# Optimization experiments

Hardware: AMD Instinct MI355X
Metric: run time of the kernel (lower is better)

Reference implementation:

```python
import jax, jax.numpy as jnp
import numpy as np

DIM = 192
TDIM = 192
HEADS = 6
WS = (2, 7, 7)
SS = (1, 3, 3)
MLP_HID = 4 * DIM
RANK = DIM // 8
EPS = 1e-6


def _rel_pos_index(ws):
    wd, wh, ww = ws
    coords = np.stack(np.meshgrid(np.arange(wd), np.arange(wh), np.arange(ww), indexing='ij'))
    cf = coords.reshape(3, -1)
    rel = (cf[:, :, None] - cf[:, None, :]).transpose(1, 2, 0).astype(np.int64)
    rel[..., 0] += wd - 1
    rel[..., 1] += wh - 1
    rel[..., 2] += ww - 1
    rel[..., 0] *= (2 * wh - 1) * (2 * ww - 1)
    rel[..., 1] *= (2 * ww - 1)
    return rel.sum(-1)  # (N, N)


def _window_partition(x, ws):
    B, D, H, W, C = x.shape
    x = x.reshape(B, D // ws[0], ws[0], H // ws[1], ws[1], W // ws[2], ws[2], C)
    return x.transpose(0, 1, 3, 5, 2, 4, 6, 7).reshape(-1, ws[0] * ws[1] * ws[2], C)


def _window_reverse(w, ws, B, D, H, W):
    x = w.reshape(B, D // ws[0], H // ws[1], W // ws[2], ws[0], ws[1], ws[2], -1)
    return x.transpose(0, 1, 4, 2, 5, 3, 6, 7).reshape(B, D, H, W, -1)


def _ln(x):
    m = x.mean(-1, keepdims=True)
    v = ((x - m) ** 2).mean(-1, keepdims=True)
    return (x - m) * jax.lax.rsqrt(v + EPS)


def _compute_mask_np(Dp, Hp, Wp, ws, ss):
    img = np.zeros((1, Dp, Hp, Wp, 1), dtype=np.float32)
    cnt = 0
    for d in (slice(0, -ws[0]), slice(-ws[0], -ss[0]), slice(-ss[0], None)):
        for h in (slice(0, -ws[1]), slice(-ws[1], -ss[1]), slice(-ss[1], None)):
            for w in (slice(0, -ws[2]), slice(-ws[2], -ss[2]), slice(-ss[2], None)):
                img[:, d, h, w, :] = cnt
                cnt += 1
    x = img.reshape(1, Dp // ws[0], ws[0], Hp // ws[1], ws[1], Wp // ws[2], ws[2], 1)
    mw = x.transpose(0, 1, 3, 5, 2, 4, 6, 7).reshape(-1, ws[0] * ws[1] * ws[2])
    am = mw[:, None, :] - mw[:, :, None]
    return np.where(am != 0, np.float32(-100.0), np.float32(0.0))


def setup_inputs() -> dict:
    key = jax.random.key(0)
    ks = jax.random.split(key, 16)
    B, D, H, W, C = 1, 16, 64, 128, DIM
    Dp = D + (-D) % WS[0]
    Hp = H + (-H) % WS[1]
    Wp = W + (-W) % WS[2]
    s = 0.02
    bias_tab = (2 * WS[0] - 1) * (2 * WS[1] - 1) * (2 * WS[2] - 1)
    return {
        'x': jax.random.normal(ks[0], (B, D, H, W, C), jnp.float32),
        'mask_matrix': jnp.asarray(_compute_mask_np(Dp, Hp, Wp, WS, SS)),
        't': jax.random.normal(ks[1], (B, TDIM), jnp.float32),
        'w_qkv': jax.random.normal(ks[2], (C, 3 * C), jnp.float32) * s,
        'b_qkv': jnp.zeros((3 * C,), jnp.float32),
        'rel_bias': jax.random.normal(ks[3], (bias_tab, HEADS), jnp.float32) * s,
        'w_proj': jax.random.normal(ks[4], (C, C), jnp.float32) * s,
        'b_proj': jnp.zeros((C,), jnp.float32),
        'w1': jax.random.normal(ks[5], (C, MLP_HID), jnp.float32) * s,
        'b1': jnp.zeros((MLP_HID,), jnp.float32),
        'w2': jax.random.normal(ks[6], (MLP_HID, C), jnp.float32) * s,
        'b2': jnp.zeros((C,), jnp.float32),
        'wa1': jax.random.normal(ks[7], (TDIM, RANK), jnp.float32) * s,
        'wa2': jax.random.normal(ks[8], (RANK, 6 * C), jnp.float32) * s,
        'ba2': jax.random.normal(ks[9], (6 * C,), jnp.float32) * s,
    }


def reference(x, mask_matrix, t, w_qkv, b_qkv, rel_bias, w_proj, b_proj, w1, b1, w2, b2, wa1, wa2, ba2):
    B, D, H, W, C = x.shape
    hd = C // HEADS
    # AdaLN modulation params
    mod = (jax.nn.silu(t) @ wa1) @ wa2 + ba2  # (B, 6C)
    sh_msa, sc_msa, g_msa, sh_mlp, sc_mlp, g_mlp = jnp.split(mod, 6, axis=1)

    def modulate(y, sh, sc):
        return y * (1 + sc[:, None, None, None, :]) + sh[:, None, None, None, :]

    shortcut = x
    y = modulate(_ln(x), sh_msa, sc_msa)
    # pad to window multiples
    pad_d, pad_h, pad_w = (-D) % WS[0], (-H) % WS[1], (-W) % WS[2]
    y = jnp.pad(y, ((0, 0), (0, pad_d), (0, pad_h), (0, pad_w), (0, 0)))
    Dp, Hp, Wp = D + pad_d, H + pad_h, W + pad_w
    # cyclic shift
    y = jnp.roll(y, (-SS[0], -SS[1], -SS[2]), axis=(1, 2, 3))
    xw = _window_partition(y, WS)  # (B*nW, N, C)
    N = xw.shape[1]
    qkv = (xw @ w_qkv + b_qkv).reshape(-1, N, 3, HEADS, hd)
    q, k, v = qkv[:, :, 0], qkv[:, :, 1], qkv[:, :, 2]
    scale = hd ** -0.5
    attn = jnp.einsum('bnhd,bmhd->bhnm', q * scale, k)  # (B*nW, H, N, N)
    rpi = _rel_pos_index(WS)
    bias = rel_bias[rpi.reshape(-1)].reshape(N, N, HEADS).transpose(2, 0, 1)
    attn = attn + bias[None]
    nW = mask_matrix.shape[0]
    attn = attn.reshape(B, nW, HEADS, N, N) + mask_matrix[None, :, None]
    attn = jax.nn.softmax(attn, axis=-1).reshape(-1, HEADS, N, N)
    out = jnp.einsum('bhnm,bmhd->bnhd', attn, v).reshape(-1, N, C)
    out = out @ w_proj + b_proj
    y = _window_reverse(out, WS, B, Dp, Hp, Wp)
    y = jnp.roll(y, (SS[0], SS[1], SS[2]), axis=(1, 2, 3))
    y = y[:, :D, :H, :W, :]
    x1 = shortcut + g_msa[:, None, None, None, :] * y
    y2 = modulate(_ln(x1), sh_mlp, sc_mlp)
    h = jax.nn.gelu(y2 @ w1 + b1, approximate=False) @ w2 + b2
    return x1 + g_mlp[:, None, None, None, :] * h
```

## Files before the change

### kernel.cpp

```cpp
#include <hip/hip_runtime.h>
#include <hip/hip_bf16.h>

typedef __bf16 bf16x8 __attribute__((ext_vector_type(8)));
typedef float  f32x4  __attribute__((ext_vector_type(4)));
typedef unsigned int u32x4 __attribute__((ext_vector_type(4)));

__device__ inline unsigned short f2bf(float f) {
    union { __hip_bfloat16 h; unsigned short u; } cv;
    cv.h = __float2bfloat16(f);
    return cv.u;
}
__device__ inline float bf2f(unsigned short u) {
    union { unsigned int i; float f; } c; c.i = ((unsigned int)u) << 16; return c.f;
}

__device__ inline bf16x8 load8(const unsigned short* p) {
    uint2 lo = *(const uint2*)(p);
    uint2 hi = *(const uint2*)(p + 16);
    u32x4 v; v[0] = lo.x; v[1] = lo.y; v[2] = hi.x; v[3] = hi.y;
    return __builtin_bit_cast(bf16x8, v);
}

__device__ inline f32x4 mfma16(bf16x8 a, bf16x8 b, f32x4 c) {
    return __builtin_amdgcn_mfma_f32_16x16x32_bf16(a, b, c, 0, 0, 0);
}

__device__ inline bool winmapT(int gg, int& T) {
    int win = gg / 98, n = gg % 98;
    int wdi = win / 190, rem = win % 190, whi = rem / 19, wwi = rem % 19;
    int td = n / 49, th = (n / 7) % 7, tw = n % 7;
    int sd = (wdi * 2 + td + 1) & 15;
    int sh = whi * 7 + th + 3; if (sh >= 70) sh -= 70;
    int sw = wwi * 7 + tw + 3; if (sw >= 133) sw -= 133;
    if (sh < 64 && sw < 128) { T = (sd * 64 + sh) * 128 + sw; return true; }
    return false;
}

__device__ inline int xcd_swz(int orig, int nwg) {
    int q = nwg >> 3, r = nwg & 7;
    int xcd = orig & 7, idx = orig >> 3;
    return (xcd < r ? xcd * (q + 1) : r * (q + 1) + (xcd - r) * q) + idx;
}

__global__ __launch_bounds__(256) void mod_k(const float* __restrict__ t,
    const float* __restrict__ wa1, const float* __restrict__ wa2,
    const float* __restrict__ ba2, float* __restrict__ mod)
{
    __shared__ float st[192];
    __shared__ float a[24];
    int tid = threadIdx.x;
    if (tid < 192) { float x = t[tid]; st[tid] = x / (1.f + __expf(-x)); }
    __syncthreads();
    if (tid < 24) {
        float s = 0.f;
        for (int c = 0; c < 192; ++c) s += st[c] * wa1[c * 24 + tid];
        a[tid] = s;
    }
    __syncthreads();
    for (int j = tid; j < 1152; j += 256) {
        float s = ba2[j];
        for (int r = 0; r < 24; ++r) s += a[r] * wa2[r * 1152 + j];
        mod[j] = s;
    }
}

__global__ __launch_bounds__(256) void prep_k(
    const float* __restrict__ wqkv, const float* __restrict__ wproj,
    const float* __restrict__ w1, const float* __restrict__ w2,
    const float* __restrict__ relb,
    unsigned short* __restrict__ wqkvT, unsigned short* __restrict__ wprojT,
    unsigned short* __restrict__ w1T, unsigned short* __restrict__ w2T,
    unsigned short* __restrict__ btabF)
{
    int i = blockIdx.x * 256 + threadIdx.x;
    if (i < 110592) { int n = i / 192, k = i % 192; wqkvT[i] = f2bf(wqkv[k * 576 + n]); return; }
    i -= 110592;
    if (i < 36864)  { int n = i / 192, k = i % 192; wprojT[i] = f2bf(wproj[k * 192 + n]); return; }
    i -= 36864;
    if (i < 147456) { int n = i / 192, k = i % 192; w1T[i] = f2bf(w1[k * 768 + n]); return; }
    i -= 147456;
    if (i < 147456) { int n = i / 768, k = i % 768; w2T[i] = f2bf(w2[k * 192 + n]); return; }
    i -= 147456;
    if (i < 688128) {
        int mt = i / 86016, r1 = i % 86016;
        int h  = r1 / 14336, r2 = r1 % 14336;
        int fq = r2 / 2048,  r3 = r2 % 2048;
        int l16 = r3 / 128,  r4 = r3 % 128;
        int lg  = r4 / 32,   r5 = r4 % 32;
        int fkey = r5 / 4,   e  = r5 % 4;
        int q = fq * 16 + l16, key = fkey * 16 + lg * 4 + e;
        float val;
        if (fkey == 7 || q >= 98 || key >= 98) {
            val = -1e30f;
        } else {
            int tdn = q / 49, thn = (q / 7) % 7, twn = q % 7;
            int tdm = key / 49, thm = (key / 7) % 7, twm = key % 7;
            int idx = (tdn - tdm + 1) * 169 + (thn - thm + 6) * 13 + (twn - twm + 6);
            float b = relb[idx * 6 + h];
            int bd = mt & 1, bh = (mt >> 1) & 1, bw = (mt >> 2) & 1;
            int idn = (bd ? (tdn == 0 ? 1 : 2) : 0) * 9 + (bh ? (thn < 4 ? 1 : 2) : 0) * 3 + (bw ? (twn < 4 ? 1 : 2) : 0);
            int idm = (bd ? (tdm == 0 ? 1 : 2) : 0) * 9 + (bh ? (thm < 4 ? 1 : 2) : 0) * 3 + (bw ? (twm < 4 ? 1 : 2) : 0);
            val = b + ((idn != idm) ? -100.f : 0.f);
        }
        btabF[i] = f2bf(val);
    }
}

__global__ __launch_bounds__(256) void lnwin_k(const float* __restrict__ x,
    const float* __restrict__ mod, unsigned short* __restrict__ ywin)
{
    int tok = blockIdx.x * 4 + (threadIdx.x >> 6);
    int lane = threadIdx.x & 63;
    int T;
    size_t ob = (size_t)tok * 192;
    if (winmapT(tok, T)) {
        const float* p = x + (size_t)T * 192;
        float x0 = p[lane], xa = p[64 + lane], xb = p[128 + lane];
        float s = x0 + xa + xb, q = x0 * x0 + xa * xa + xb * xb;
        for (int m = 32; m; m >>= 1) { s += __shfl_xor(s, m); q += __shfl_xor(q, m); }
        float mean = s * (1.f / 192.f);
        float var  = q * (1.f / 192.f) - mean * mean;
        float rstd = rsqrtf(var + 1e-6f);
        ywin[ob + lane]       = f2bf((x0 - mean) * rstd * (1.f + mod[192 + lane])       + mod[lane]);
        ywin[ob + 64 + lane]  = f2bf((xa - mean) * rstd * (1.f + mod[192 + 64 + lane])  + mod[64 + lane]);
        ywin[ob + 128 + lane] = f2bf((xb - mean) * rstd * (1.f + mod[192 + 128 + lane]) + mod[128 + lane]);
    } else {
        ywin[ob + lane] = 0; ywin[ob + 64 + lane] = 0; ywin[ob + 128 + lane] = 0;
    }
}

__global__ __launch_bounds__(256) void ln2_k(const float* __restrict__ x1,
    const float* __restrict__ mod, unsigned short* __restrict__ y2)
{
    int tok = blockIdx.x * 4 + (threadIdx.x >> 6);
    int lane = threadIdx.x & 63;
    const float* p = x1 + (size_t)tok * 192;
    float x0 = p[lane], xa = p[64 + lane], xb = p[128 + lane];
    float s = x0 + xa + xb, q = x0 * x0 + xa * xa + xb * xb;
    for (int m = 32; m; m >>= 1) { s += __shfl_xor(s, m); q += __shfl_xor(q, m); }
    float mean = s * (1.f / 192.f);
    float var  = q * (1.f / 192.f) - mean * mean;
    float rstd = rsqrtf(var + 1e-6f);
    size_t ob = (size_t)tok * 192;
    y2[ob + lane]       = f2bf((x0 - mean) * rstd * (1.f + mod[768 + lane])       + mod[576 + lane]);
    y2[ob + 64 + lane]  = f2bf((xa - mean) * rstd * (1.f + mod[768 + 64 + lane])  + mod[576 + 64 + lane]);
    y2[ob + 128 + lane] = f2bf((xb - mean) * rstd * (1.f + mod[768 + 128 + lane]) + mod[576 + 128 + lane]);
}

template<int FN, int EPI>
__global__ __launch_bounds__(256) void gemm_k(
    const unsigned short* __restrict__ A, const unsigned short* __restrict__ BT,
    const float* __restrict__ bias, unsigned short* __restrict__ outB, float* outF,
    const float* __restrict__ auxF, const float* __restrict__ mod,
    int M, int N, int K, int nx)
{
    constexpr int BN = FN * 32;
    __shared__ unsigned short As[128][40];
    __shared__ unsigned short Bs[BN][40];
    const int t = threadIdx.x;
    const int wg = xcd_swz(blockIdx.x, gridDim.x);
    const int n0 = (wg % nx) * BN, m0 = (wg / nx) * 128;
    const int lr = t >> 2, lk = (t & 3) * 8;
    const int wid = t >> 6, lane = t & 63;
    const int lg = lane >> 4, l16 = lane & 15;
    const int wm = (wid >> 1) * 64, wn = (wid & 1) * (FN * 16);
    f32x4 acc[4][FN] = {};

    for (int kk = 0; kk < K; kk += 32) {
        #pragma unroll
        for (int rr = 0; rr < 2; ++rr) {
            int r = lr + rr * 64;
            int g = m0 + r;
            uint4 w = make_uint4(0u, 0u, 0u, 0u);
            if (g < M) w = *(const uint4*)(A + (size_t)g * K + kk + lk);
            *(uint4*)(&As[r][lk]) = w;
        }
        #pragma unroll
        for (int rr = 0; rr < BN / 64; ++rr) {
            int r = lr + rr * 64;
            int gn = n0 + r;
            uint4 w = make_uint4(0u, 0u, 0u, 0u);
            if (gn < N) w = *(const uint4*)(BT + (size_t)gn * K + kk + lk);
            *(uint4*)(&Bs[r][lk]) = w;
        }
        __syncthreads();
        bf16x8 af[4], bv[FN];
        #pragma unroll
        for (int i = 0; i < 4; ++i) af[i] = load8(&As[wm + i * 16 + l16][4 * lg]);
        #pragma unroll
        for (int j = 0; j < FN; ++j) bv[j] = load8(&Bs[wn + j * 16 + l16][4 * lg]);
        #pragma unroll
        for (int i = 0; i < 4; ++i)
        #pragma unroll
        for (int j = 0; j < FN; ++j)
            acc[i][j] = mfma16(af[i], bv[j], acc[i][j]);
        __syncthreads();
    }

    #pragma unroll
    for (int i = 0; i < 4; ++i)
    #pragma unroll
    for (int j = 0; j < FN; ++j) {
        int gcol = n0 + wn + j * 16 + l16;
        if (gcol >= N) continue;
        float b = bias[gcol];
        #pragma unroll
        for (int e = 0; e < 4; ++e) {
            int grow = m0 + wm + i * 16 + lg * 4 + e;
            if (grow >= M) continue;
            float v = acc[i][j][e] + b;
            if (EPI == 0) {
                int which = gcol / 192, hh = (gcol / 32) % 6, c = gcol & 31;
                outB[((size_t)(hh * 3 + which) * 148960 + grow) * 32 + c] = f2bf(v);
            } else if (EPI == 1) {
                float gl = 0.5f * v * (1.f + erff(v * 0.70710678118654752f));
                outB[(size_t)grow * N + gcol] = f2bf(gl);
            } else if (EPI == 2) {
                int T;
                if (winmapT(grow, T)) {
                    size_t idx = (size_t)T * 192 + gcol;
                    outF[idx] = auxF[idx] + mod[384 + gcol] * v;
                }
            } else {
                size_t idx = (size_t)grow * 192 + gcol;
                outF[idx] = outF[idx] + mod[960 + gcol] * v;
            }
        }
    }
}

__global__ __launch_bounds__(256) void attn_k(
    const unsigned short* __restrict__ qkv, const unsigned short* __restrict__ btabF,
    unsigned short* __restrict__ out)
{
    __shared__ __align__(16) unsigned short Ks[112 * 46];
    __shared__ __align__(16) unsigned short VT[32 * 142];

    const int wg = xcd_swz(blockIdx.x, 9120);
    const int h = wg / 1520, win = wg % 1520;
    const int t = threadIdx.x;
    const int wid = t >> 6, lg = (t >> 4) & 3, l16 = t & 15;
    const size_t rb = (size_t)win * 98;

    const unsigned short* Qg = qkv + (size_t)(h * 3 + 0) * 148960 * 32;
    const unsigned short* Kg = qkv + (size_t)(h * 3 + 1) * 148960 * 32;
    const unsigned short* Vg = qkv + (size_t)(h * 3 + 2) * 148960 * 32;

    const int wdi = win / 190, remw = win % 190, whi = remw / 19, wwi = remw % 19;
    const int mt = (wdi == 7 ? 1 : 0) | (whi == 9 ? 2 : 0) | (wwi == 18 ? 4 : 0);
    const unsigned short* btF = btabF + (size_t)(mt * 6 + h) * 14336;

    bf16x8 qa[2];
    uint4 btr[2][4];
    #pragma unroll
    for (int fi = 0; fi < 2; ++fi) {
        int fq = wid + fi * 4;
        int fqc = (fq < 7) ? fq : 0;
        qa[fi] = load8(Qg + (rb + fqc * 16 + l16) * 32 + 4 * lg);
        const uint4* bp = (const uint4*)(btF + fqc * 2048 + l16 * 128 + lg * 32);
        btr[fi][0] = bp[0]; btr[fi][1] = bp[1]; btr[fi][2] = bp[2]; btr[fi][3] = bp[3];
    }

    for (int i = t; i < 392; i += 256) {
        int r = i >> 2, cg = (i & 3) * 8;
        uint4 k = *(const uint4*)(Kg + (rb + r) * 32 + cg);
        *(uint2*)(Ks + r * 46 + cg)     = make_uint2(k.x, k.y);
        *(uint2*)(Ks + r * 46 + cg + 4) = make_uint2(k.z, k.w);
    }
    for (int i = t; i < 14 * 32; i += 256) {
        int r = 98 + (i >> 5), c = i & 31;
        Ks[r * 46 + c] = 0;
    }
    if (t < 392) {
        uint4 v = *(const uint4*)(Vg + (rb + (t >> 2)) * 32 + (t & 3) * 8);
        const unsigned short* vp = (const unsigned short*)&v;
        int m = t >> 2, c0 = (t & 3) * 8;
        #pragma unroll
        for (int j = 0; j < 8; ++j) VT[(c0 + j) * 142 + m] = vp[j];
    }
    {
        int t2 = t + 256;
        if (t2 < 392) {
            uint4 v = *(const uint4*)(Vg + (rb + (t2 >> 2)) * 32 + (t2 & 3) * 8);
            const unsigned short* vp = (const unsigned short*)&v;
            int m = t2 >> 2, c0 = (t2 & 3) * 8;
            #pragma unroll
            for (int j = 0; j < 8; ++j) VT[(c0 + j) * 142 + m] = vp[j];
        }
    }
    for (int i = t; i < 32 * 30; i += 256) { int c = i / 30, m = 98 + i % 30; VT[c * 142 + m] = 0; }
    __syncthreads();

    __builtin_amdgcn_s_setprio(1);
    const float SCALE = 0.17677669529663687f;
    #pragma unroll
    for (int fi = 0; fi < 2; ++fi) {
        const int fq = wid + fi * 4;
        if (fq >= 7) break;

        const unsigned bt32[16] = {btr[fi][0].x, btr[fi][0].y, btr[fi][0].z, btr[fi][0].w,
                                   btr[fi][1].x, btr[fi][1].y, btr[fi][1].z, btr[fi][1].w,
                                   btr[fi][2].x, btr[fi][2].y, btr[fi][2].z, btr[fi][2].w,
                                   btr[fi][3].x, btr[fi][3].y, btr[fi][3].z, btr[fi][3].w};

        f32x4 acc[7];
        #pragma unroll
        for (int fk = 0; fk < 7; ++fk) {
            bf16x8 kb = load8(Ks + (fk * 16 + l16) * 46 + 4 * lg);
            f32x4 z = {};
            acc[fk] = mfma16(kb, qa[fi], z);
        }

        float mx = -1e30f;
        #pragma unroll
        for (int fk = 0; fk < 7; ++fk)
        #pragma unroll
        for (int e = 0; e < 4; ++e) {
            unsigned short bu = (unsigned short)(bt32[fk * 2 + (e >> 1)] >> ((e & 1) * 16));
            float s = fmaf(acc[fk][e], SCALE, bf2f(bu));
            acc[fk][e] = s;
            mx = fmaxf(mx, s);
        }
        mx = fmaxf(mx, __shfl_xor(mx, 16));
        mx = fmaxf(mx, __shfl_xor(mx, 32));
        float sum = 0.f;
        #pragma unroll
        for (int fk = 0; fk < 7; ++fk)
        #pragma unroll
        for (int e = 0; e < 4; ++e) {
            float p = __expf(acc[fk][e] - mx);
            acc[fk][e] = p;
            sum += p;
        }
        sum += __shfl_xor(sum, 16);
        sum += __shfl_xor(sum, 32);
        float rinv = 1.f / sum;

        bf16x8 sa[4];
        #pragma unroll
        for (int ks = 0; ks < 4; ++ks) {
            u32x4 w;
            w[0] = (unsigned)f2bf(acc[2 * ks][0]) | ((unsigned)f2bf(acc[2 * ks][1]) << 16);
            w[1] = (unsigned)f2bf(acc[2 * ks][2]) | ((unsigned)f2bf(acc[2 * ks][3]) << 16);
            if (ks < 3) {
                w[2] = (unsigned)f2bf(acc[2 * ks + 1][0]) | ((unsigned)f2bf(acc[2 * ks + 1][1]) << 16);
                w[3] = (unsigned)f2bf(acc[2 * ks + 1][2]) | ((unsigned)f2bf(acc[2 * ks + 1][3]) << 16);
            } else {
                w[2] = 0u; w[3] = 0u;
            }
            sa[ks] = __builtin_bit_cast(bf16x8, w);
        }
        float rv[4];
        #pragma unroll
        for (int e = 0; e < 4; ++e) rv[e] = __shfl(rinv, lg * 4 + e);

        #pragma unroll
        for (int fn = 0; fn < 2; ++fn) {
            f32x4 o = {};
            #pragma unroll
            for (int ks = 0; ks < 4; ++ks) {
                bf16x8 vb = load8(VT + (fn * 16 + l16) * 142 + ks * 32 + 4 * lg);
                o = mfma16(sa[ks], vb, o);
            }
            #pragma unroll
            for (int e = 0; e < 4; ++e) {
                int r = fq * 16 + lg * 4 + e;
                if (r < 98) {
                    out[(rb + r) * 192 + h * 32 + fn * 16 + l16] = f2bf(o[e] * rv[e]);
                }
            }
        }
    }
    __builtin_amdgcn_s_setprio(0);
}

extern "C" void kernel_launch(void* const* d_in, const int* in_sizes, int n_in,
                              void* d_out, int out_size, void* d_ws, size_t ws_size,
                              hipStream_t stream)
{
    const float* x      = (const float*)d_in[0];
    const float* tvec   = (const float*)d_in[2];
    const float* w_qkv  = (const float*)d_in[3];
    const float* b_qkv  = (const float*)d_in[4];
    const float* relb   = (const float*)d_in[5];
    const float* w_proj = (const float*)d_in[6];
    const float* b_proj = (const float*)d_in[7];
    const float* w1     = (const float*)d_in[8];
    const float* b1     = (const float*)d_in[9];
    const float* w2     = (const float*)d_in[10];
    const float* b2     = (const float*)d_in[11];
    const float* wa1    = (const float*)d_in[12];
    const float* wa2    = (const float*)d_in[13];
    const float* ba2    = (const float*)d_in[14];

    char* ws = (char*)d_ws;
    float*          mod    = (float*)ws;
    unsigned short* wqkvT  = (unsigned short*)(ws + 2101760);
    unsigned short* wprojT = (unsigned short*)(ws + 2322944);
    unsigned short* w1T    = (unsigned short*)(ws + 2396672);
    unsigned short* w2T    = (unsigned short*)(ws + 2691584);
    unsigned short* btabF  = (unsigned short*)(ws + 2986496);
    unsigned short* qkvb   = (unsigned short*)(ws + 4834304);
    unsigned short* h      = (unsigned short*)(ws + 4834304);
    unsigned short* attn_c = (unsigned short*)(ws + 176436224);
    unsigned short* ywin   = (unsigned short*)(ws + 233636864);
    unsigned short* y2b    = (unsigned short*)(ws + 290837504);
    float*          dout   = (float*)d_out;

    mod_k<<<1, 256, 0, stream>>>(tvec, wa1, wa2, ba2, mod);
    prep_k<<<4416, 256, 0, stream>>>(w_qkv, w_proj, w1, w2, relb, wqkvT, wprojT, w1T, w2T, btabF);
    lnwin_k<<<37240, 256, 0, stream>>>(x, mod, ywin);

    gemm_k<4, 0><<<5 * 1164, 256, 0, stream>>>(
        ywin, wqkvT, b_qkv, qkvb, nullptr, nullptr, mod, 148960, 576, 192, 5);
    attn_k<<<9120, 256, 0, stream>>>(qkvb, btabF, attn_c);
    gemm_k<2, 2><<<3 * 1164, 256, 0, stream>>>(
        attn_c, wprojT, b_proj, nullptr, dout, x, mod, 148960, 192, 192, 3);

    ln2_k<<<32768, 256, 0, stream>>>(dout, mod, y2b);

    gemm_k<4, 1><<<6 * 1024, 256, 0, stream>>>(
        y2b, w1T, b1, h, nullptr, nullptr, mod, 131072, 768, 192, 6);
    gemm_k<2, 3><<<3 * 1024, 256, 0, stream>>>(
        h, w2T, b2, nullptr, dout, nullptr, mod, 131072, 192, 768, 3);
}
```

Before: 950.6 us.

## Use direct global-to-LDS loads with XOR swizzle in GEMM; two windows per attention block

The GEMM tile loads now use global_load_lds to copy A and B tiles straight into LDS, dropping the register round trip and the padded layout. Row chunks are XOR-swizzled so fragment reads avoid bank conflicts. The attention kernel now handles two windows per block, one per pair of waves, halving the grid, and loads the bias table inside the loop instead of prefetching it. This trades more LDS per block and more work per wave for fewer blocks and cheaper GEMM staging.

```diff
diff --git a/kernel.cpp b/kernel.cpp
--- a/kernel.cpp
+++ b/kernel.cpp
@@ -4,6 +4,8 @@
 typedef __bf16 bf16x8 __attribute__((ext_vector_type(8)));
 typedef float  f32x4  __attribute__((ext_vector_type(4)));
 typedef unsigned int u32x4 __attribute__((ext_vector_type(4)));
+typedef __attribute__((address_space(3))) unsigned int lds_u32;
+typedef const __attribute__((address_space(1))) unsigned int glb_u32;
 
 __device__ inline unsigned short f2bf(float f) {
     union { __hip_bfloat16 h; unsigned short u; } cv;
@@ -17,6 +19,15 @@
 __device__ inline bf16x8 load8(const unsigned short* p) {
     uint2 lo = *(const uint2*)(p);
     uint2 hi = *(const uint2*)(p + 16);
+    u32x4 v; v[0] = lo.x; v[1] = lo.y; v[2] = hi.x; v[3] = hi.y;
+    return __builtin_bit_cast(bf16x8, v);
+}
+
+__device__ inline bf16x8 load8s(const unsigned short* rowbase, int lg, int r3) {
+    int b0 = ((((lg >> 1)    ) ^ r3) << 4) + ((lg & 1) << 3);
+    int b1 = ((((lg >> 1) + 2) ^ r3) << 4) + ((lg & 1) << 3);
+    uint2 lo = *(const uint2*)((const char*)rowbase + b0);
+    uint2 hi = *(const uint2*)((const char*)rowbase + b1);
     u32x4 v; v[0] = lo.x; v[1] = lo.y; v[2] = hi.x; v[3] = hi.y;
     return __builtin_bit_cast(bf16x8, v);
 }
@@ -155,40 +166,51 @@
     int M, int N, int K, int nx)
 {
     constexpr int BN = FN * 32;
-    __shared__ unsigned short As[128][40];
-    __shared__ unsigned short Bs[BN][40];
+    __shared__ unsigned short As[128 * 32];
+    __shared__ unsigned short Bs[BN * 32];
     const int t = threadIdx.x;
     const int wg = xcd_swz(blockIdx.x, gridDim.x);
     const int n0 = (wg % nx) * BN, m0 = (wg / nx) * 128;
-    const int lr = t >> 2, lk = (t & 3) * 8;
     const int wid = t >> 6, lane = t & 63;
     const int lg = lane >> 4, l16 = lane & 15;
     const int wm = (wid >> 1) * 64, wn = (wid & 1) * (FN * 16);
     f32x4 acc[4][FN] = {};
 
+    int arow[2], acs[2];
+    #pragma unroll
+    for (int j = 0; j < 2; ++j) {
+        int p = t + j * 256;
+        arow[j] = p >> 2;
+        acs[j] = (p & 3) ^ (arow[j] & 3);
+    }
+
     for (int kk = 0; kk < K; kk += 32) {
         #pragma unroll
-        for (int rr = 0; rr < 2; ++rr) {
-            int r = lr + rr * 64;
-            int g = m0 + r;
-            uint4 w = make_uint4(0u, 0u, 0u, 0u);
-            if (g < M) w = *(const uint4*)(A + (size_t)g * K + kk + lk);
-            *(uint4*)(&As[r][lk]) = w;
-        }
-        #pragma unroll
-        for (int rr = 0; rr < BN / 64; ++rr) {
-            int r = lr + rr * 64;
-            int gn = n0 + r;
-            uint4 w = make_uint4(0u, 0u, 0u, 0u);
-            if (gn < N) w = *(const uint4*)(BT + (size_t)gn * K + kk + lk);
-            *(uint4*)(&Bs[r][lk]) = w;
+        for (int j = 0; j < 2; ++j) {
+            int gr = m0 + arow[j];
+            const unsigned short* src = A + (size_t)(gr < M ? gr : 0) * K + kk + acs[j] * 8;
+            __builtin_amdgcn_global_load_lds((glb_u32*)src,
+                (lds_u32*)((char*)As + wid * 1024 + j * 4096), 16, 0, 0);
+        }
+        #pragma unroll
+        for (int j = 0; j < BN / 64; ++j) {
+            int gn = n0 + arow[j];
+            const unsigned short* src = BT + (size_t)(gn < N ? gn : 0) * K + kk + acs[j] * 8;
+            __builtin_amdgcn_global_load_lds((glb_u32*)src,
+                (lds_u32*)((char*)Bs + wid * 1024 + j * 4096), 16, 0, 0);
         }
         __syncthreads();
         bf16x8 af[4], bv[FN];
         #pragma unroll
-        for (int i = 0; i < 4; ++i) af[i] = load8(&As[wm + i * 16 + l16][4 * lg]);
-        #pragma unroll
-        for (int j = 0; j < FN; ++j) bv[j] = load8(&Bs[wn + j * 16 + l16][4 * lg]);
+        for (int i = 0; i < 4; ++i) {
+            int r = wm + i * 16 + l16;
+            af[i] = load8s(As + r * 32, lg, r & 3);
+        }
+        #pragma unroll
+        for (int j = 0; j < FN; ++j) {
+            int r = wn + j * 16 + l16;
+            bv[j] = load8s(Bs + r * 32, lg, r & 3);
+        }
         #pragma unroll
         for (int i = 0; i < 4; ++i)
         #pragma unroll
@@ -233,82 +255,84 @@
     const unsigned short* __restrict__ qkv, const unsigned short* __restrict__ btabF,
     unsigned short* __restrict__ out)
 {
-    __shared__ __align__(16) unsigned short Ks[112 * 46];
-    __shared__ __align__(16) unsigned short VT[32 * 142];
-
-    const int wg = xcd_swz(blockIdx.x, 9120);
-    const int h = wg / 1520, win = wg % 1520;
+    __shared__ __align__(16) unsigned short Ks[2][112 * 46];
+    __shared__ __align__(16) unsigned short VT[2][32 * 142];
+
+    const int wg = xcd_swz(blockIdx.x, 4560);
+    const int h = wg / 760, wp = wg % 760;
+    const int win0 = wp * 2;
     const int t = threadIdx.x;
     const int wid = t >> 6, lg = (t >> 4) & 3, l16 = t & 15;
-    const size_t rb = (size_t)win * 98;
 
     const unsigned short* Qg = qkv + (size_t)(h * 3 + 0) * 148960 * 32;
     const unsigned short* Kg = qkv + (size_t)(h * 3 + 1) * 148960 * 32;
     const unsigned short* Vg = qkv + (size_t)(h * 3 + 2) * 148960 * 32;
 
+    const int w2 = wid & 1, fq0 = wid >> 1;
+    const int win = win0 + w2;
+    const size_t rb = (size_t)win * 98;
     const int wdi = win / 190, remw = win % 190, whi = remw / 19, wwi = remw % 19;
     const int mt = (wdi == 7 ? 1 : 0) | (whi == 9 ? 2 : 0) | (wwi == 18 ? 4 : 0);
-    const unsigned short* btF = btabF + (size_t)(mt * 6 + h) * 14336;
-
-    bf16x8 qa[2];
-    uint4 btr[2][4];
-    #pragma unroll
-    for (int fi = 0; fi < 2; ++fi) {
-        int fq = wid + fi * 4;
+    const unsigned short* btW = btabF + (size_t)(mt * 6 + h) * 14336;
+
+    bf16x8 qa[4];
+    #pragma unroll
+    for (int i = 0; i < 4; ++i) {
+        int fq = fq0 + 2 * i;
         int fqc = (fq < 7) ? fq : 0;
-        qa[fi] = load8(Qg + (rb + fqc * 16 + l16) * 32 + 4 * lg);
-        const uint4* bp = (const uint4*)(btF + fqc * 2048 + l16 * 128 + lg * 32);
-        btr[fi][0] = bp[0]; btr[fi][1] = bp[1]; btr[fi][2] = bp[2]; btr[fi][3] = bp[3];
-    }
-
-    for (int i = t; i < 392; i += 256) {
-        int r = i >> 2, cg = (i & 3) * 8;
-        uint4 k = *(const uint4*)(Kg + (rb + r) * 32 + cg);
-        *(uint2*)(Ks + r * 46 + cg)     = make_uint2(k.x, k.y);
-        *(uint2*)(Ks + r * 46 + cg + 4) = make_uint2(k.z, k.w);
-    }
-    for (int i = t; i < 14 * 32; i += 256) {
-        int r = 98 + (i >> 5), c = i & 31;
-        Ks[r * 46 + c] = 0;
-    }
-    if (t < 392) {
-        uint4 v = *(const uint4*)(Vg + (rb + (t >> 2)) * 32 + (t & 3) * 8);
-        const unsigned short* vp = (const unsigned short*)&v;
-        int m = t >> 2, c0 = (t & 3) * 8;
-        #pragma unroll
-        for (int j = 0; j < 8; ++j) VT[(c0 + j) * 142 + m] = vp[j];
-    }
-    {
-        int t2 = t + 256;
-        if (t2 < 392) {
-            uint4 v = *(const uint4*)(Vg + (rb + (t2 >> 2)) * 32 + (t2 & 3) * 8);
-            const unsigned short* vp = (const unsigned short*)&v;
-            int m = t2 >> 2, c0 = (t2 & 3) * 8;
-            #pragma unroll
-            for (int j = 0; j < 8; ++j) VT[(c0 + j) * 142 + m] = vp[j];
-        }
-    }
-    for (int i = t; i < 32 * 30; i += 256) { int c = i / 30, m = 98 + i % 30; VT[c * 142 + m] = 0; }
+        qa[i] = load8(Qg + (rb + fqc * 16 + l16) * 32 + 4 * lg);
+    }
+
+    #pragma unroll
+    for (int v2 = 0; v2 < 2; ++v2) {
+        const size_t rbs = (size_t)(win0 + v2) * 98;
+        for (int i = t; i < 392; i += 256) {
+            int r = i >> 2, cg = (i & 3) * 8;
+            uint4 k = *(const uint4*)(Kg + (rbs + r) * 32 + cg);
+            *(uint2*)(&Ks[v2][r * 46 + cg])     = make_uint2(k.x, k.y);
+            *(uint2*)(&Ks[v2][r * 46 + cg + 4]) = make_uint2(k.z, k.w);
+        }
+        for (int i = t; i < 14 * 32; i += 256) {
+            int r = 98 + (i >> 5), c = i & 31;
+            Ks[v2][r * 46 + c] = 0;
+        }
+        for (int i = t; i < 512; i += 256) {
+            if (i < 392) {
+                uint4 v = *(const uint4*)(Vg + (rbs + (i >> 2)) * 32 + (i & 3) * 8);
+                const unsigned short* vp = (const unsigned short*)&v;
+                int m = i >> 2, c0 = (i & 3) * 8;
+                #pragma unroll
+                for (int j = 0; j < 8; ++j) VT[v2][(c0 + j) * 142 + m] = vp[j];
+            }
+        }
+        for (int i = t; i < 32 * 30; i += 256) {
+            int c = i / 30, m = 98 + i % 30;
+            VT[v2][c * 142 + m] = 0;
+        }
+    }
     __syncthreads();
 
     __builtin_amdgcn_s_setprio(1);
     const float SCALE = 0.17677669529663687f;
-    #pragma unroll
-    for (int fi = 0; fi < 2; ++fi) {
-        const int fq = wid + fi * 4;
+    const unsigned short* KsW = &Ks[w2][0];
+    const unsigned short* VTW = &VT[w2][0];
+
+    #pragma unroll
+    for (int i = 0; i < 4; ++i) {
+        const int fq = fq0 + 2 * i;
         if (fq >= 7) break;
 
-        const unsigned bt32[16] = {btr[fi][0].x, btr[fi][0].y, btr[fi][0].z, btr[fi][0].w,
-                                   btr[fi][1].x, btr[fi][1].y, btr[fi][1].z, btr[fi][1].w,
-                                   btr[fi][2].x, btr[fi][2].y, btr[fi][2].z, btr[fi][2].w,
-                                   btr[fi][3].x, btr[fi][3].y, btr[fi][3].z, btr[fi][3].w};
+        const uint4* bp = (const uint4*)(btW + fq * 2048 + l16 * 128 + lg * 32);
+        uint4 b0 = bp[0], b1 = bp[1], b2 = bp[2], b3 = bp[3];
+        const unsigned bt32[16] = {b0.x, b0.y, b0.z, b0.w, b1.x, b1.y, b1.z, b1.w,
+                                   b2.x, b2.y, b2.z, b2.w, b3.x, b3.y, b3.z, b3.w};
 
         f32x4 acc[7];
         #pragma unroll
         for (int fk = 0; fk < 7; ++fk) {
-            bf16x8 kb = load8(Ks + (fk * 16 + l16) * 46 + 4 * lg);
+            bf16x8 kb = load8(KsW + (fk * 16 + l16) * 46 + 4 * lg);
             f32x4 z = {};
-            acc[fk] = mfma16(kb, qa[fi], z);
+            acc[fk] = mfma16(kb, qa[i], z);
         }
 
         float mx = -1e30f;
@@ -359,7 +383,7 @@
             f32x4 o = {};
             #pragma unroll
             for (int ks = 0; ks < 4; ++ks) {
-                bf16x8 vb = load8(VT + (fn * 16 + l16) * 142 + ks * 32 + 4 * lg);
+                bf16x8 vb = load8(VTW + (fn * 16 + l16) * 142 + ks * 32 + 4 * lg);
                 o = mfma16(sa[ks], vb, o);
             }
             #pragma unroll
@@ -413,7 +437,7 @@
 
     gemm_k<4, 0><<<5 * 1164, 256, 0, stream>>>(
         ywin, wqkvT, b_qkv, qkvb, nullptr, nullptr, mod, 148960, 576, 192, 5);
-    attn_k<<<9120, 256, 0, stream>>>(qkvb, btabF, attn_c);
+    attn_k<<<4560, 256, 0, stream>>>(qkvb, btabF, attn_c);
     gemm_k<2, 2><<<3 * 1164, 256, 0, stream>>>(
         attn_c, wprojT, b_proj, nullptr, dout, x, mod, 148960, 192, 192, 3);
 
```

Result: no change. 957.1 us (+0.7%).
